# Performance work log

Hardware: AMD Instinct MI355X
Metric: run time of the kernel (lower is better)

The kernel has to match this reference:

```python
import jax, jax.numpy as jnp
import numpy as np

SEQ_LEN = 2048
N_FFT = 4096  # nearest power of two >= 2*SEQ_LEN - 1
K = 24
D_IN = 512
D_OUT = 512
K_U = 3


def setup_inputs() -> dict:
    key = jax.random.key(0)
    k1, k2, k3, k4, k5 = jax.random.split(key, 5)
    x = jax.random.normal(k1, (1, SEQ_LEN, D_IN), dtype=jnp.float32)
    phi = jax.random.normal(k2, (SEQ_LEN, K), dtype=jnp.float32)
    M = jax.random.normal(k3, (D_OUT, D_IN, K_U), dtype=jnp.float32) / D_IN
    M_phi_plus = jax.random.normal(k4, (K, D_IN, D_OUT), dtype=jnp.float32) / 10.0
    M_phi_minus = jax.random.normal(k5, (K, D_IN, D_OUT), dtype=jnp.float32) / 10.0
    return {"x": x, "phi": phi, "M": M, "M_phi_plus": M_phi_plus, "M_phi_minus": M_phi_minus}


def _convolve(u, v, n):
    # u: (bsz, seq, d_in); v: (seq, K) spectral filters
    bsz, seq_len, d_in = u.shape
    Kf = v.shape[1]
    # alternating sign (+1, -1, +1, ...) along time, shape (1, seq, 1, 1)
    sgn = jnp.where(jnp.arange(seq_len) % 2 == 1, -1.0, 1.0).reshape(1, seq_len, 1, 1)
    v_f = jnp.fft.rfft(v.astype(jnp.float32).reshape(1, seq_len, Kf, 1, 1), n=n, axis=1)
    u_exp = jnp.broadcast_to(u[:, :, None, :], (bsz, seq_len, Kf, d_in))
    # stack [u, u*sgn] -> (bsz, seq, K, d_in, 2)
    U = jnp.stack([u_exp, u_exp * sgn], axis=-1).astype(jnp.float32)
    U_f = jnp.fft.rfft(U, n=n, axis=1)
    U_conv = jnp.fft.irfft(v_f * U_f, n=n, axis=1)[:, :seq_len]
    U_plus = U_conv[..., 0]
    U_minus = U_conv[..., 1] * sgn  # (b, seq, K, d_in) * (1, seq, 1, 1)
    return U_plus, U_minus


def _ar_preds(M, x):
    # M: (d_out, d_in, k_u); x: (b, l, d_in)
    # ar[t] = sum_{i=0}^{k_u-1} M[:,:,i] @ x[t-i]  (zero before start)
    b, l, _ = x.shape
    out = jnp.zeros((b, l, M.shape[0]), dtype=x.dtype)
    for i in range(M.shape[-1]):
        x_shift = jnp.pad(x, ((0, 0), (i, 0), (0, 0)))[:, :l]
        out = out + jnp.einsum("bli,oi->blo", x_shift, M[:, :, i])
    return out


def reference(x, phi, M, M_phi_plus, M_phi_minus):
    U_plus, U_minus = _convolve(x, phi, N_FFT)
    spectral_plus = jnp.einsum("blkd,kdo->blo", U_plus, M_phi_plus)
    spectral_minus = jnp.einsum("blkd,kdo->blo", U_minus, M_phi_minus)
    output = spectral_plus + spectral_minus  # use_hankel_L=False
    ar = _ar_preds(M, x)
    return output + ar
```

## Files before the change

### kernel.cpp

```cpp
#include <hip/hip_runtime.h>

typedef __bf16 bf16;
typedef bf16 bf16x8 __attribute__((ext_vector_type(8)));
typedef float floatx16 __attribute__((ext_vector_type(16)));

#define AS1 __attribute__((address_space(1)))
#define AS3 __attribute__((address_space(3)))

#define KTOT 26112

__device__ __forceinline__ void stage_tile(const bf16* g, int ld, bf16* lds, int tid) {
#pragma unroll
    for (int it = 0; it < 4; ++it) {
        int q    = it * 256 + tid;
        int row  = q >> 3;
        int col8 = (q & 7) ^ (row & 7);
        __builtin_amdgcn_global_load_lds(
            (const AS1 void*)(g + (size_t)row * ld + col8 * 8),
            (AS3 void*)(lds + q * 8), 16, 0, 0);
    }
}

__device__ __forceinline__ void mfma_block(const bf16* lA, const bf16* lB,
                                           floatx16 acc[2][2], int lane, int wm, int wn) {
    const int lrow = lane & 31;
    const int lk   = lane >> 5;
#pragma unroll
    for (int s = 0; s < 4; ++s) {
        bf16x8 af[2], bfr[2];
        const int c8 = s * 2 + lk;
#pragma unroll
        for (int mi = 0; mi < 2; ++mi) {
            int r = wm * 64 + mi * 32 + lrow;
            af[mi] = *(const bf16x8*)(lA + r * 64 + ((c8 ^ (r & 7)) << 3));
        }
#pragma unroll
        for (int ni = 0; ni < 2; ++ni) {
            int r = wn * 64 + ni * 32 + lrow;
            bfr[ni] = *(const bf16x8*)(lB + r * 64 + ((c8 ^ (r & 7)) << 3));
        }
#pragma unroll
        for (int mi = 0; mi < 2; ++mi)
#pragma unroll
            for (int ni = 0; ni < 2; ++ni)
                acc[mi][ni] = __builtin_amdgcn_mfma_f32_32x32x16_bf16(
                    af[mi], bfr[ni], acc[mi][ni], 0, 0, 0);
    }
}

#define CD_ROW(r, lane) (((r) & 3) + 8 * ((r) >> 2) + 4 * ((lane) >> 5))

__global__ __launch_bounds__(256) void conv_gemm(const bf16* __restrict__ Tb,
                                                 const bf16* __restrict__ xT,
                                                 bf16* __restrict__ A2) {
    __shared__ bf16 lA[128 * 64], lB[128 * 64];
    const int tid = threadIdx.x;
    const int lane = tid & 63, wave = tid >> 6, wm = wave & 1, wn = wave >> 1;
    const int bid = blockIdx.x;
    const int a    = 15 - (bid / 192);
    const int rem  = bid % 192;
    const int kf   = rem >> 2;
    const int dblk = rem & 3;

    floatx16 acc[2][2];
#pragma unroll
    for (int mi = 0; mi < 2; ++mi)
#pragma unroll
        for (int ni = 0; ni < 2; ++ni)
#pragma unroll
            for (int e = 0; e < 16; ++e) acc[mi][ni][e] = 0.f;

    for (int c = 0; c <= a; ++c) {
        const bf16* Ab = Tb + ((size_t)kf * 16 + (a - c)) * 16384;
        const bf16* Bb = xT + (size_t)(dblk * 128) * 2048 + c * 128;
#pragma unroll
        for (int kk = 0; kk < 128; kk += 64) {
            stage_tile(Ab + kk, 128, lA, tid);
            stage_tile(Bb + kk, 2048, lB, tid);
            __syncthreads();
            mfma_block(lA, lB, acc, lane, wm, wn);
            __syncthreads();
        }
    }
    bf16* Ob = A2 + (size_t)(a * 128) * KTOT + kf * 512 + dblk * 128;
#pragma unroll
    for (int mi = 0; mi < 2; ++mi)
#pragma unroll
        for (int ni = 0; ni < 2; ++ni)
#pragma unroll
            for (int r = 0; r < 16; ++r) {
                int row = wm * 64 + mi * 32 + CD_ROW(r, lane);
                int col = wn * 64 + ni * 32 + (lane & 31);
                Ob[(size_t)row * KTOT + col] = (bf16)acc[mi][ni][r];
            }
}

__global__ __launch_bounds__(256) void proj_gemm(const bf16* __restrict__ A2,
                                                 const bf16* __restrict__ B2,
                                                 float* __restrict__ P2) {
    __shared__ bf16 lA[128 * 64], lB[128 * 64];
    const int tid = threadIdx.x;
    const int lane = tid & 63, wave = tid >> 6, wm = wave & 1, wn = wave >> 1;
    const int bm = blockIdx.x, sp = blockIdx.y, bn = blockIdx.z;
    const bf16* Ab = A2 + (size_t)bm * 128 * KTOT + sp * 2176;
    const bf16* Bb = B2 + (size_t)bn * 128 * KTOT + sp * 2176;

    floatx16 acc[2][2];
#pragma unroll
    for (int mi = 0; mi < 2; ++mi)
#pragma unroll
        for (int ni = 0; ni < 2; ++ni)
#pragma unroll
            for (int e = 0; e < 16; ++e) acc[mi][ni][e] = 0.f;

    for (int kk = 0; kk < 2176; kk += 64) {
        stage_tile(Ab + kk, KTOT, lA, tid);
        stage_tile(Bb + kk, KTOT, lB, tid);
        __syncthreads();
        mfma_block(lA, lB, acc, lane, wm, wn);
        __syncthreads();
    }
    float* Pt = P2 + (size_t)sp * 1048576;
#pragma unroll
    for (int mi = 0; mi < 2; ++mi)
#pragma unroll
        for (int ni = 0; ni < 2; ++ni)
#pragma unroll
            for (int r = 0; r < 16; ++r) {
                int t = bm * 128 + wm * 64 + mi * 32 + CD_ROW(r, lane);
                int o = bn * 128 + wn * 64 + ni * 32 + (lane & 31);
                Pt[(size_t)t * 512 + o] = acc[mi][ni][r];
            }
}

__global__ void prep_all(const float* __restrict__ x, const float* __restrict__ phi,
                         const float* __restrict__ M, const float* __restrict__ Mp,
                         const float* __restrict__ Mm, bf16* __restrict__ xT,
                         bf16* __restrict__ A2, bf16* __restrict__ B2,
                         bf16* __restrict__ Tb) {
    __shared__ float smem[64 * 65];
    const int b = blockIdx.x, tid = threadIdx.x;
    if (b < 256) {
        int tt = (b >> 3) * 64, dd = (b & 7) * 64;
#pragma unroll
        for (int it = 0; it < 16; ++it) {
            int q = it * 256 + tid;
            int r = q >> 6, cc = q & 63;
            smem[r * 65 + cc] = x[(size_t)(tt + r) * 512 + dd + cc];
        }
        __syncthreads();
#pragma unroll
        for (int it = 0; it < 16; ++it) {
            int q = it * 256 + tid;
            int r = q >> 6, cc = q & 63;
            xT[(size_t)(dd + r) * 2048 + tt + cc] = (bf16)smem[cc * 65 + r];
        }
    } else if (b < 1792) {
        int idx8 = (b - 256) * 256 + tid;
        int t = idx8 / 192, q = idx8 % 192;
        int i = q >> 6, d8 = (q & 63) * 8;
        bf16x8 v;
        if (t - i >= 0) {
            const float* xp = x + (size_t)(t - i) * 512 + d8;
#pragma unroll
            for (int jj = 0; jj < 8; ++jj) v[jj] = (bf16)xp[jj];
        } else {
#pragma unroll
            for (int jj = 0; jj < 8; ++jj) v[jj] = (bf16)0.f;
        }
        *(bf16x8*)(A2 + (size_t)t * KTOT + 24576 + i * 512 + d8) = v;
    } else if (b < 4864) {
        int b2 = b - 1792;
        int kv = b2 >> 6, rem = b2 & 63;
        int dt = (rem >> 3) * 64, ot = (rem & 7) * 64;
        const float* src = (kv < 24) ? (Mp + (size_t)kv * 262144)
                                     : (Mm + (size_t)(kv - 24) * 262144);
#pragma unroll
        for (int it = 0; it < 16; ++it) {
            int q = it * 256 + tid;
            int r = q >> 6, cc = q & 63;
            smem[r * 65 + cc] = src[(size_t)(dt + r) * 512 + ot + cc];
        }
        __syncthreads();
#pragma unroll
        for (int it = 0; it < 16; ++it) {
            int q = it * 256 + tid;
            int r = q >> 6, cc = q & 63;
            B2[(size_t)(ot + r) * KTOT + kv * 512 + dt + cc] = (bf16)smem[cc * 65 + r];
        }
    } else if (b < 5376) {
        int o = b - 4864;
        for (int q = tid; q < 1536; q += 256) smem[q] = M[(size_t)o * 1536 + q];
        __syncthreads();
        for (int q = tid; q < 1536; q += 256) {
            int i = q >> 9, d = q & 511;
            B2[(size_t)o * KTOT + 24576 + q] = (bf16)smem[d * 3 + i];
        }
    } else {
        int b3 = b - 5376;
        int kv = b3 >> 4, m = b3 & 15;
        int k  = (kv >= 24) ? kv - 24 : kv;
        if (tid < 255) {
            int sh = m * 128 - 127 + tid;
            float f = 0.f;
            if (sh >= 0) {
                f = phi[sh * 24 + k];
                if (kv >= 24 && (sh & 1)) f = -f;
            }
            smem[tid] = f;
        }
        __syncthreads();
        bf16* Tp = Tb + (size_t)b3 * 16384;
#pragma unroll
        for (int it = 0; it < 8; ++it) {
            int q = it * 256 + tid;
            int i = q >> 4, j8 = (q & 15) * 8;
            bf16x8 v;
#pragma unroll
            for (int jj = 0; jj < 8; ++jj)
                v[jj] = (bf16)smem[127 + i - (j8 + jj)];
            *(bf16x8*)(Tp + i * 128 + j8) = v;
        }
    }
}

__global__ void reduce12(const float* __restrict__ P2, float* __restrict__ out) {
    int idx = blockIdx.x * 256 + threadIdx.x;
    if (idx >= 2048 * 512) return;
    float s = 0.f;
#pragma unroll
    for (int sp = 0; sp < 12; ++sp)
        s += P2[(size_t)sp * 1048576 + idx];
    out[idx] = s;
}

extern "C" void kernel_launch(void* const* d_in, const int* in_sizes, int n_in,
                              void* d_out, int out_size, void* d_ws, size_t ws_size,
                              hipStream_t stream) {
    const float* x   = (const float*)d_in[0];
    const float* phi = (const float*)d_in[1];
    const float* M   = (const float*)d_in[2];
    const float* Mp  = (const float*)d_in[3];
    const float* Mm  = (const float*)d_in[4];
    float* out = (float*)d_out;
    char* ws = (char*)d_ws;

    bf16*  Tb = (bf16*)(ws + 0);
    bf16*  xT = (bf16*)(ws + 25165824);
    bf16*  A2 = (bf16*)(ws + 27262976);
    bf16*  B2 = (bf16*)(ws + 134217728);
    float* P2 = (float*)(ws + 160956416);

    prep_all<<<6144, 256, 0, stream>>>(x, phi, M, Mp, Mm, xT, A2, B2, Tb);
    conv_gemm<<<3072, 256, 0, stream>>>(Tb, xT, A2);
    proj_gemm<<<dim3(16, 12, 4), 256, 0, stream>>>(A2, B2, P2);
    reduce12<<<4096, 256, 0, stream>>>(P2, out);
}
```

Measured before the change: 297.7 us.

## Fuse weight prep into conv GEMM launch and raise projection split-K to 17

Moves the projection-weight transpose and autoregressive input packing out of the prep kernel into extra blocks of the convolution GEMM launch, so this memory-bound work can fill CUs left idle by the triangular conv workload. The projection GEMM split-K count rises from 12 to 17 slices, increasing block count for better occupancy. In exchange, the reduce step reads more partial sums and more fp32 partials are written to workspace.

```diff
diff --git a/kernel.cpp b/kernel.cpp
--- a/kernel.cpp
+++ b/kernel.cpp
@@ -50,94 +50,8 @@
 
 #define CD_ROW(r, lane) (((r) & 3) + 8 * ((r) >> 2) + 4 * ((lane) >> 5))
 
-__global__ __launch_bounds__(256) void conv_gemm(const bf16* __restrict__ Tb,
-                                                 const bf16* __restrict__ xT,
-                                                 bf16* __restrict__ A2) {
-    __shared__ bf16 lA[128 * 64], lB[128 * 64];
-    const int tid = threadIdx.x;
-    const int lane = tid & 63, wave = tid >> 6, wm = wave & 1, wn = wave >> 1;
-    const int bid = blockIdx.x;
-    const int a    = 15 - (bid / 192);
-    const int rem  = bid % 192;
-    const int kf   = rem >> 2;
-    const int dblk = rem & 3;
-
-    floatx16 acc[2][2];
-#pragma unroll
-    for (int mi = 0; mi < 2; ++mi)
-#pragma unroll
-        for (int ni = 0; ni < 2; ++ni)
-#pragma unroll
-            for (int e = 0; e < 16; ++e) acc[mi][ni][e] = 0.f;
-
-    for (int c = 0; c <= a; ++c) {
-        const bf16* Ab = Tb + ((size_t)kf * 16 + (a - c)) * 16384;
-        const bf16* Bb = xT + (size_t)(dblk * 128) * 2048 + c * 128;
-#pragma unroll
-        for (int kk = 0; kk < 128; kk += 64) {
-            stage_tile(Ab + kk, 128, lA, tid);
-            stage_tile(Bb + kk, 2048, lB, tid);
-            __syncthreads();
-            mfma_block(lA, lB, acc, lane, wm, wn);
-            __syncthreads();
-        }
-    }
-    bf16* Ob = A2 + (size_t)(a * 128) * KTOT + kf * 512 + dblk * 128;
-#pragma unroll
-    for (int mi = 0; mi < 2; ++mi)
-#pragma unroll
-        for (int ni = 0; ni < 2; ++ni)
-#pragma unroll
-            for (int r = 0; r < 16; ++r) {
-                int row = wm * 64 + mi * 32 + CD_ROW(r, lane);
-                int col = wn * 64 + ni * 32 + (lane & 31);
-                Ob[(size_t)row * KTOT + col] = (bf16)acc[mi][ni][r];
-            }
-}
-
-__global__ __launch_bounds__(256) void proj_gemm(const bf16* __restrict__ A2,
-                                                 const bf16* __restrict__ B2,
-                                                 float* __restrict__ P2) {
-    __shared__ bf16 lA[128 * 64], lB[128 * 64];
-    const int tid = threadIdx.x;
-    const int lane = tid & 63, wave = tid >> 6, wm = wave & 1, wn = wave >> 1;
-    const int bm = blockIdx.x, sp = blockIdx.y, bn = blockIdx.z;
-    const bf16* Ab = A2 + (size_t)bm * 128 * KTOT + sp * 2176;
-    const bf16* Bb = B2 + (size_t)bn * 128 * KTOT + sp * 2176;
-
-    floatx16 acc[2][2];
-#pragma unroll
-    for (int mi = 0; mi < 2; ++mi)
-#pragma unroll
-        for (int ni = 0; ni < 2; ++ni)
-#pragma unroll
-            for (int e = 0; e < 16; ++e) acc[mi][ni][e] = 0.f;
-
-    for (int kk = 0; kk < 2176; kk += 64) {
-        stage_tile(Ab + kk, KTOT, lA, tid);
-        stage_tile(Bb + kk, KTOT, lB, tid);
-        __syncthreads();
-        mfma_block(lA, lB, acc, lane, wm, wn);
-        __syncthreads();
-    }
-    float* Pt = P2 + (size_t)sp * 1048576;
-#pragma unroll
-    for (int mi = 0; mi < 2; ++mi)
-#pragma unroll
-        for (int ni = 0; ni < 2; ++ni)
-#pragma unroll
-            for (int r = 0; r < 16; ++r) {
-                int t = bm * 128 + wm * 64 + mi * 32 + CD_ROW(r, lane);
-                int o = bn * 128 + wn * 64 + ni * 32 + (lane & 31);
-                Pt[(size_t)t * 512 + o] = acc[mi][ni][r];
-            }
-}
-
-__global__ void prep_all(const float* __restrict__ x, const float* __restrict__ phi,
-                         const float* __restrict__ M, const float* __restrict__ Mp,
-                         const float* __restrict__ Mm, bf16* __restrict__ xT,
-                         bf16* __restrict__ A2, bf16* __restrict__ B2,
-                         bf16* __restrict__ Tb) {
+__global__ void prep1(const float* __restrict__ x, const float* __restrict__ phi,
+                      bf16* __restrict__ xT, bf16* __restrict__ Tb) {
     __shared__ float smem[64 * 65];
     const int b = blockIdx.x, tid = threadIdx.x;
     if (b < 256) {
@@ -155,49 +69,8 @@
             int r = q >> 6, cc = q & 63;
             xT[(size_t)(dd + r) * 2048 + tt + cc] = (bf16)smem[cc * 65 + r];
         }
-    } else if (b < 1792) {
-        int idx8 = (b - 256) * 256 + tid;
-        int t = idx8 / 192, q = idx8 % 192;
-        int i = q >> 6, d8 = (q & 63) * 8;
-        bf16x8 v;
-        if (t - i >= 0) {
-            const float* xp = x + (size_t)(t - i) * 512 + d8;
-#pragma unroll
-            for (int jj = 0; jj < 8; ++jj) v[jj] = (bf16)xp[jj];
-        } else {
-#pragma unroll
-            for (int jj = 0; jj < 8; ++jj) v[jj] = (bf16)0.f;
-        }
-        *(bf16x8*)(A2 + (size_t)t * KTOT + 24576 + i * 512 + d8) = v;
-    } else if (b < 4864) {
-        int b2 = b - 1792;
-        int kv = b2 >> 6, rem = b2 & 63;
-        int dt = (rem >> 3) * 64, ot = (rem & 7) * 64;
-        const float* src = (kv < 24) ? (Mp + (size_t)kv * 262144)
-                                     : (Mm + (size_t)(kv - 24) * 262144);
-#pragma unroll
-        for (int it = 0; it < 16; ++it) {
-            int q = it * 256 + tid;
-            int r = q >> 6, cc = q & 63;
-            smem[r * 65 + cc] = src[(size_t)(dt + r) * 512 + ot + cc];
-        }
-        __syncthreads();
-#pragma unroll
-        for (int it = 0; it < 16; ++it) {
-            int q = it * 256 + tid;
-            int r = q >> 6, cc = q & 63;
-            B2[(size_t)(ot + r) * KTOT + kv * 512 + dt + cc] = (bf16)smem[cc * 65 + r];
-        }
-    } else if (b < 5376) {
-        int o = b - 4864;
-        for (int q = tid; q < 1536; q += 256) smem[q] = M[(size_t)o * 1536 + q];
-        __syncthreads();
-        for (int q = tid; q < 1536; q += 256) {
-            int i = q >> 9, d = q & 511;
-            B2[(size_t)o * KTOT + 24576 + q] = (bf16)smem[d * 3 + i];
-        }
     } else {
-        int b3 = b - 5376;
+        int b3 = b - 256;
         int kv = b3 >> 4, m = b3 & 15;
         int k  = (kv >= 24) ? kv - 24 : kv;
         if (tid < 255) {
@@ -224,12 +97,146 @@
     }
 }
 
-__global__ void reduce12(const float* __restrict__ P2, float* __restrict__ out) {
+__global__ __launch_bounds__(256) void conv_fused(const bf16* __restrict__ Tb,
+                                                  const bf16* __restrict__ xT,
+                                                  bf16* __restrict__ A2,
+                                                  const float* __restrict__ x,
+                                                  const float* __restrict__ M,
+                                                  const float* __restrict__ Mp,
+                                                  const float* __restrict__ Mm,
+                                                  bf16* __restrict__ B2) {
+    __shared__ float4 raw4[2048];
+    const int bid = blockIdx.x, tid = threadIdx.x;
+    if (bid < 3072) {
+        bf16* lA = (bf16*)raw4;
+        bf16* lB = (bf16*)raw4 + 128 * 64;
+        const int lane = tid & 63, wave = tid >> 6, wm = wave & 1, wn = wave >> 1;
+        const int a    = 15 - (bid / 192);
+        const int rem  = bid % 192;
+        const int kf   = rem >> 2;
+        const int dblk = rem & 3;
+
+        floatx16 acc[2][2];
+#pragma unroll
+        for (int mi = 0; mi < 2; ++mi)
+#pragma unroll
+            for (int ni = 0; ni < 2; ++ni)
+#pragma unroll
+                for (int e = 0; e < 16; ++e) acc[mi][ni][e] = 0.f;
+
+        for (int c = 0; c <= a; ++c) {
+            const bf16* Ab = Tb + ((size_t)kf * 16 + (a - c)) * 16384;
+            const bf16* Bb = xT + (size_t)(dblk * 128) * 2048 + c * 128;
+#pragma unroll
+            for (int kk = 0; kk < 128; kk += 64) {
+                stage_tile(Ab + kk, 128, lA, tid);
+                stage_tile(Bb + kk, 2048, lB, tid);
+                __syncthreads();
+                mfma_block(lA, lB, acc, lane, wm, wn);
+                __syncthreads();
+            }
+        }
+        bf16* Ob = A2 + (size_t)(a * 128) * KTOT + kf * 512 + dblk * 128;
+#pragma unroll
+        for (int mi = 0; mi < 2; ++mi)
+#pragma unroll
+            for (int ni = 0; ni < 2; ++ni)
+#pragma unroll
+                for (int r = 0; r < 16; ++r) {
+                    int row = wm * 64 + mi * 32 + CD_ROW(r, lane);
+                    int col = wn * 64 + ni * 32 + (lane & 31);
+                    Ob[(size_t)row * KTOT + col] = (bf16)acc[mi][ni][r];
+                }
+    } else if (bid < 6144) {
+        float* smem = (float*)raw4;
+        int b2 = bid - 3072;
+        int kv = b2 >> 6, rem = b2 & 63;
+        int dt = (rem >> 3) * 64, ot = (rem & 7) * 64;
+        const float* src = (kv < 24) ? (Mp + (size_t)kv * 262144)
+                                     : (Mm + (size_t)(kv - 24) * 262144);
+#pragma unroll
+        for (int it = 0; it < 16; ++it) {
+            int q = it * 256 + tid;
+            int r = q >> 6, cc = q & 63;
+            smem[r * 65 + cc] = src[(size_t)(dt + r) * 512 + ot + cc];
+        }
+        __syncthreads();
+#pragma unroll
+        for (int it = 0; it < 16; ++it) {
+            int q = it * 256 + tid;
+            int r = q >> 6, cc = q & 63;
+            B2[(size_t)(ot + r) * KTOT + kv * 512 + dt + cc] = (bf16)smem[cc * 65 + r];
+        }
+    } else if (bid < 7680) {
+        int idx8 = (bid - 6144) * 256 + tid;
+        int t = idx8 / 192, q = idx8 % 192;
+        int i = q >> 6, d8 = (q & 63) * 8;
+        bf16x8 v;
+        if (t - i >= 0) {
+            const float* xp = x + (size_t)(t - i) * 512 + d8;
+#pragma unroll
+            for (int jj = 0; jj < 8; ++jj) v[jj] = (bf16)xp[jj];
+        } else {
+#pragma unroll
+            for (int jj = 0; jj < 8; ++jj) v[jj] = (bf16)0.f;
+        }
+        *(bf16x8*)(A2 + (size_t)t * KTOT + 24576 + i * 512 + d8) = v;
+    } else {
+        float* smem = (float*)raw4;
+        int o = bid - 7680;
+        for (int q = tid; q < 1536; q += 256) smem[q] = M[(size_t)o * 1536 + q];
+        __syncthreads();
+        for (int q = tid; q < 1536; q += 256) {
+            int i = q >> 9, d = q & 511;
+            B2[(size_t)o * KTOT + 24576 + q] = (bf16)smem[d * 3 + i];
+        }
+    }
+}
+
+__global__ __launch_bounds__(256) void proj_gemm(const bf16* __restrict__ A2,
+                                                 const bf16* __restrict__ B2,
+                                                 float* __restrict__ P2) {
+    __shared__ bf16 lA[128 * 64], lB[128 * 64];
+    const int tid = threadIdx.x;
+    const int lane = tid & 63, wave = tid >> 6, wm = wave & 1, wn = wave >> 1;
+    const int bm = blockIdx.x, sp = blockIdx.y, bn = blockIdx.z;
+    const bf16* Ab = A2 + (size_t)bm * 128 * KTOT + sp * 1536;
+    const bf16* Bb = B2 + (size_t)bn * 128 * KTOT + sp * 1536;
+
+    floatx16 acc[2][2];
+#pragma unroll
+    for (int mi = 0; mi < 2; ++mi)
+#pragma unroll
+        for (int ni = 0; ni < 2; ++ni)
+#pragma unroll
+            for (int e = 0; e < 16; ++e) acc[mi][ni][e] = 0.f;
+
+    for (int kk = 0; kk < 1536; kk += 64) {
+        stage_tile(Ab + kk, KTOT, lA, tid);
+        stage_tile(Bb + kk, KTOT, lB, tid);
+        __syncthreads();
+        mfma_block(lA, lB, acc, lane, wm, wn);
+        __syncthreads();
+    }
+    float* Pt = P2 + (size_t)sp * 1048576;
+#pragma unroll
+    for (int mi = 0; mi < 2; ++mi)
+#pragma unroll
+        for (int ni = 0; ni < 2; ++ni)
+#pragma unroll
+            for (int r = 0; r < 16; ++r) {
+                int t = bm * 128 + wm * 64 + mi * 32 + CD_ROW(r, lane);
+                int o = bn * 128 + wn * 64 + ni * 32 + (lane & 31);
+                Pt[(size_t)t * 512 + o] = acc[mi][ni][r];
+            }
+}
+
+__global__ void reduce17(const float* __restrict__ P2, float* __restrict__ out) {
     int idx = blockIdx.x * 256 + threadIdx.x;
     if (idx >= 2048 * 512) return;
     float s = 0.f;
 #pragma unroll
-    for (int sp = 0; sp < 12; ++sp)
+    for (int sp = 0; sp < 17; ++sp)
         s += P2[(size_t)sp * 1048576 + idx];
     out[idx] = s;
 }
@@ -251,8 +258,8 @@
     bf16*  B2 = (bf16*)(ws + 134217728);
     float* P2 = (float*)(ws + 160956416);
 
-    prep_all<<<6144, 256, 0, stream>>>(x, phi, M, Mp, Mm, xT, A2, B2, Tb);
-    conv_gemm<<<3072, 256, 0, stream>>>(Tb, xT, A2);
-    proj_gemm<<<dim3(16, 12, 4), 256, 0, stream>>>(A2, B2, P2);
-    reduce12<<<4096, 256, 0, stream>>>(P2, out);
-}
+    prep1<<<1024, 256, 0, stream>>>(x, phi, xT, Tb);
+    conv_fused<<<8192, 256, 0, stream>>>(Tb, xT, A2, x, M, Mp, Mm, B2);
+    proj_gemm<<<dim3(16, 17, 4), 256, 0, stream>>>(A2, B2, P2);
+    reduce17<<<4096, 256, 0, stream>>>(P2, out);
+}
```

Measured after the change: 346.4 us. +16.4%, slower.

## Store split-K partials in bf16, vectorize B2 transpose writes and reduction

Applied to the files above, without the earlier changes.

The split-K partial sums from the projection GEMM are now written as bf16 instead of fp32, which halves the partial buffer traffic. The reduction kernel reads eight bf16 values per thread with vector loads. The prep kernel's transposed weight writes are packed into 16-byte bf16x8 stores instead of scalar stores. Rounding the partials to bf16 before summing them adds precision loss to the output.

```diff
diff --git a/kernel.cpp b/kernel.cpp
--- a/kernel.cpp
+++ b/kernel.cpp
@@ -97,7 +97,7 @@
 
 __global__ __launch_bounds__(256) void proj_gemm(const bf16* __restrict__ A2,
                                                  const bf16* __restrict__ B2,
-                                                 float* __restrict__ P2) {
+                                                 bf16* __restrict__ P2) {
     __shared__ bf16 lA[128 * 64], lB[128 * 64];
     const int tid = threadIdx.x;
     const int lane = tid & 63, wave = tid >> 6, wm = wave & 1, wn = wave >> 1;
@@ -120,7 +120,7 @@
         mfma_block(lA, lB, acc, lane, wm, wn);
         __syncthreads();
     }
-    float* Pt = P2 + (size_t)sp * 1048576;
+    bf16* Pt = P2 + (size_t)sp * 1048576;
 #pragma unroll
     for (int mi = 0; mi < 2; ++mi)
 #pragma unroll
@@ -129,7 +129,7 @@
             for (int r = 0; r < 16; ++r) {
                 int t = bm * 128 + wm * 64 + mi * 32 + CD_ROW(r, lane);
                 int o = bn * 128 + wn * 64 + ni * 32 + (lane & 31);
-                Pt[(size_t)t * 512 + o] = acc[mi][ni][r];
+                Pt[(size_t)t * 512 + o] = (bf16)acc[mi][ni][r];
             }
 }
 
@@ -183,10 +183,14 @@
         }
         __syncthreads();
 #pragma unroll
-        for (int it = 0; it < 16; ++it) {
-            int q = it * 256 + tid;
-            int r = q >> 6, cc = q & 63;
-            B2[(size_t)(ot + r) * KTOT + kv * 512 + dt + cc] = (bf16)smem[cc * 65 + r];
+        for (int it = 0; it < 2; ++it) {
+            int q = it * 256 + tid;
+            int o = q >> 3, d8 = (q & 7) * 8;
+            bf16x8 v;
+#pragma unroll
+            for (int jj = 0; jj < 8; ++jj)
+                v[jj] = (bf16)smem[(d8 + jj) * 65 + o];
+            *(bf16x8*)(B2 + (size_t)(ot + o) * KTOT + kv * 512 + dt + d8) = v;
         }
     } else if (b < 5376) {
         int o = b - 4864;
@@ -224,14 +228,21 @@
     }
 }
 
-__global__ void reduce12(const float* __restrict__ P2, float* __restrict__ out) {
-    int idx = blockIdx.x * 256 + threadIdx.x;
-    if (idx >= 2048 * 512) return;
-    float s = 0.f;
-#pragma unroll
-    for (int sp = 0; sp < 12; ++sp)
-        s += P2[(size_t)sp * 1048576 + idx];
-    out[idx] = s;
+__global__ void reduce12(const bf16* __restrict__ P2, float* __restrict__ out) {
+    int idx8 = blockIdx.x * 256 + threadIdx.x;
+    if (idx8 >= 2048 * 64) return;
+    size_t base = (size_t)idx8 * 8;
+    float s[8];
+#pragma unroll
+    for (int jj = 0; jj < 8; ++jj) s[jj] = 0.f;
+#pragma unroll
+    for (int sp = 0; sp < 12; ++sp) {
+        bf16x8 v = *(const bf16x8*)(P2 + (size_t)sp * 1048576 + base);
+#pragma unroll
+        for (int jj = 0; jj < 8; ++jj) s[jj] += (float)v[jj];
+    }
+#pragma unroll
+    for (int jj = 0; jj < 8; ++jj) out[base + jj] = s[jj];
 }
 
 extern "C" void kernel_launch(void* const* d_in, const int* in_sizes, int n_in,
@@ -245,14 +256,14 @@
     float* out = (float*)d_out;
     char* ws = (char*)d_ws;
 
-    bf16*  Tb = (bf16*)(ws + 0);
-    bf16*  xT = (bf16*)(ws + 25165824);
-    bf16*  A2 = (bf16*)(ws + 27262976);
-    bf16*  B2 = (bf16*)(ws + 134217728);
-    float* P2 = (float*)(ws + 160956416);
+    bf16* Tb = (bf16*)(ws + 0);
+    bf16* xT = (bf16*)(ws + 25165824);
+    bf16* A2 = (bf16*)(ws + 27262976);
+    bf16* B2 = (bf16*)(ws + 134217728);
+    bf16* P2 = (bf16*)(ws + 160956416);
 
     prep_all<<<6144, 256, 0, stream>>>(x, phi, M, Mp, Mm, xT, A2, B2, Tb);
     conv_gemm<<<3072, 256, 0, stream>>>(Tb, xT, A2);
     proj_gemm<<<dim3(16, 12, 4), 256, 0, stream>>>(A2, B2, P2);
-    reduce12<<<4096, 256, 0, stream>>>(P2, out);
-}
+    reduce12<<<512, 256, 0, stream>>>(P2, out);
+}
```

Result: slower. 308.4 us (+3.6%).
